# Kernel tuning notes

Measured on AMD Instinct MI355X. Metric: run time of the kernel, lower is better.

Reference implementation:

```python
import jax, jax.numpy as jnp
import numpy as np

N, E, D, L = 50000, 800000, 128, 3
BN_EPS = 1e-5

def setup_inputs() -> dict:
    key = jax.random.key(0)
    ks = jax.random.split(key, 6)
    x = jax.random.normal(ks[0], (N, D), dtype=jnp.float32)
    edge_index = jax.random.randint(ks[1], (2, E), 0, N, dtype=jnp.int64)
    W1 = jax.random.normal(ks[2], (L, D, D), dtype=jnp.float32) * (1.0 / np.sqrt(D))
    W2 = jax.random.normal(ks[3], (L, D, D), dtype=jnp.float32) * (1.0 / np.sqrt(D))
    return {
        'x': x, 'edge_index': edge_index,
        'W1': W1, 'b1': jnp.zeros((L, D), jnp.float32),
        'gamma': jnp.ones((L, D), jnp.float32), 'beta': jnp.zeros((L, D), jnp.float32),
        'bn_mean': jnp.zeros((L, D), jnp.float32), 'bn_var': jnp.ones((L, D), jnp.float32),
        'W2': W2, 'b2': jnp.zeros((L, D), jnp.float32),
        'eps': jnp.zeros((L,), jnp.float32),
    }

def reference(x, edge_index, W1, b1, gamma, beta, bn_mean, bn_var, W2, b2, eps):
    src, dst = edge_index[0], edge_index[1]
    h = x
    for l in range(L):
        # GIN aggregation: (1+eps)*h_i + sum_{j->i} h_j  (scatter-add over edges)
        agg = jax.ops.segment_sum(h[src], dst, num_segments=N)  # [N, D]
        z = (1.0 + eps[l]) * h + agg
        # MLP: Linear -> BatchNorm(eval, running stats) -> ReLU -> Linear
        z = z @ W1[l] + b1[l]
        z = (z - bn_mean[l]) * jax.lax.rsqrt(bn_var[l] + BN_EPS) * gamma[l] + beta[l]
        z = jax.nn.relu(z)
        z = z @ W2[l] + b2[l]
        if l < L - 1:
            z = jax.nn.relu(z)  # inter-layer ReLU; dropout is identity in eval
        h = z
    return h
```

## Files before the change

### kernel.cpp

```cpp
#include <hip/hip_runtime.h>
#include <hip/hip_fp16.h>

#define NN 50000
#define NE 800000
#define DD 128
#define NL 3
#define BN_EPS 1e-5f

#define NBIN 196
#define BCAP 5120
#define EB 4096
#define NB3 ((NE + EB - 1) / EB)

typedef short bf16x8 __attribute__((ext_vector_type(8)));
typedef float f32x4  __attribute__((ext_vector_type(4)));
typedef unsigned int u32x4 __attribute__((ext_vector_type(4)));


__device__ __forceinline__ unsigned int rne16(float v) {
    unsigned int u = __float_as_uint(v);
    return (u + 0x7fffu + ((u >> 16) & 1u)) >> 16;
}
__device__ __forceinline__ unsigned int packf(float v) {
    unsigned int hb = rne16(v);
    float hf = __uint_as_float(hb << 16);
    unsigned int lb = rne16(v - hf);
    return (hb << 16) | lb;
}
__device__ __forceinline__ float unpackf(unsigned int p) {
    return __uint_as_float(p & 0xffff0000u) + __uint_as_float(p << 16);
}


__global__ __launch_bounds__(256) void binscatter_kernel(
    const int* __restrict__ src, const int* __restrict__ dst,
    int* __restrict__ bin_cursor, uint2* __restrict__ binned) {
    __shared__ int lhist[NBIN];
    __shared__ int lbase[NBIN];
    __shared__ int lcur[NBIN];
    int t = threadIdx.x;
    for (int i = t; i < NBIN; i += 256) { lhist[i] = 0; lcur[i] = 0; }
    __syncthreads();
    int base = blockIdx.x * EB;
    int d[16], s[16], b[16];
#pragma unroll
    for (int i = 0; i < 16; ++i) {
        int e = base + t + i * 256;
        if (e < NE) {
            d[i] = dst[e]; s[i] = src[e]; b[i] = d[i] >> 8;
            atomicAdd(&lhist[b[i]], 1);
        } else b[i] = -1;
    }
    __syncthreads();
    for (int i = t; i < NBIN; i += 256) {
        int c = lhist[i];
        lbase[i] = c ? atomicAdd(&bin_cursor[i], c) : 0;
    }
    __syncthreads();
#pragma unroll
    for (int i = 0; i < 16; ++i)
        if (b[i] >= 0) {
            int p = lbase[b[i]] + atomicAdd(&lcur[b[i]], 1);
            binned[(size_t)b[i] * BCAP + p] = make_uint2((unsigned)s[i], (unsigned)d[i]);
        }
}

__global__ __launch_bounds__(256) void bincount_kernel(
    const uint2* __restrict__ binned, const int* __restrict__ bin_cursor,
    int* __restrict__ counts) {
    __shared__ int lcnt[256];
    int bI = blockIdx.x, t = threadIdx.x;
    lcnt[t] = 0;
    __syncthreads();
    int cnt = bin_cursor[bI];
    const uint2* be = binned + (size_t)bI * BCAP;
    for (int i = t; i < cnt; i += 256)
        atomicAdd(&lcnt[be[i].y & 255], 1);
    __syncthreads();
    int node = bI * 256 + t;
    if (node < NN) counts[node] = lcnt[t];
}

__global__ void scan1_kernel(const int* __restrict__ counts, int* __restrict__ otmp,
                             int* __restrict__ bsums) {
    __shared__ int sd[1024];
    int t = threadIdx.x;
    int i = blockIdx.x * 1024 + t;
    int v = (i < NN) ? counts[i] : 0;
    sd[t] = v; __syncthreads();
    for (int off = 1; off < 1024; off <<= 1) {
        int tmp = (t >= off) ? sd[t - off] : 0;
        __syncthreads();
        sd[t] += tmp;
        __syncthreads();
    }
    if (i < NN) otmp[i] = sd[t] - v;
    if (t == 1023) bsums[blockIdx.x] = sd[1023];
}

__global__ void scan2_kernel(const int* __restrict__ bsums, int* __restrict__ boffs, int nb) {
    __shared__ int sd[64];
    int t = threadIdx.x;
    int v = (t < nb) ? bsums[t] : 0;
    sd[t] = v; __syncthreads();
    for (int off = 1; off < 64; off <<= 1) {
        int tmp = (t >= off) ? sd[t - off] : 0;
        __syncthreads();
        sd[t] += tmp;
        __syncthreads();
    }
    if (t < nb) boffs[t] = sd[t] - v;
}

__global__ void scan3_kernel(const int* __restrict__ otmp, const int* __restrict__ boffs,
                             int* __restrict__ offsets) {
    int i = blockIdx.x * 1024 + threadIdx.x;
    if (i < NN) offsets[i] = otmp[i] + boffs[blockIdx.x];
}

__global__ __launch_bounds__(256) void binfill_kernel(
    const uint2* __restrict__ binned, const int* __restrict__ bin_cursor,
    const int* __restrict__ offs, int* __restrict__ csr) {
    __shared__ int lcur[256];
    int bI = blockIdx.x, t = threadIdx.x;
    lcur[t] = 0;
    __syncthreads();
    int cnt = bin_cursor[bI];
    const uint2* be = binned + (size_t)bI * BCAP;
    for (int i = t; i < cnt; i += 256) {
        uint2 e = be[i];
        int node = (int)e.y;
        int p = atomicAdd(&lcur[node & 255], 1);
        csr[offs[node] + p] = (int)e.x;
    }
}


__global__ void wsplit_kernel(const float* __restrict__ W1, const float* __restrict__ W2,
                              unsigned short* __restrict__ Whi, unsigned short* __restrict__ Wlo) {
    int idx = blockIdx.x * 256 + threadIdx.x;
    if (idx >= 6 * 16384) return;
    int m = idx >> 14;
    int r = idx & 16383;
    int n = r >> 7, k = r & 127;
    const float* Wsrc = (m < 3) ? (W1 + (size_t)m * 16384) : (W2 + (size_t)(m - 3) * 16384);
    float v = Wsrc[k * DD + n];
    unsigned int hb = rne16(v);
    float hf = __uint_as_float(hb << 16);
    unsigned int lb = rne16(v - hf);
    Whi[idx] = (unsigned short)hb;
    Wlo[idx] = (unsigned short)lb;
}


__global__ void tofp16_kernel(const float* __restrict__ x, unsigned int* __restrict__ x16) {
    int i = blockIdx.x * 256 + threadIdx.x;
    if (i >= NN * 64) return;
    float2 v = ((const float2*)x)[i];
    __half2 h = __float22half2_rn(v);
    x16[i] = __builtin_bit_cast(unsigned int, h);
}


template <bool SELF_F32>
__global__ __launch_bounds__(256) void agg_kernel(const void* __restrict__ selfv,
    const unsigned int* __restrict__ h16,
    const int* __restrict__ offsets, const int* __restrict__ counts,
    const int* __restrict__ csr, const float* __restrict__ eps, int l,
    unsigned int* __restrict__ aggp) {
    int wid = (int)((blockIdx.x * 256 + threadIdx.x) >> 6);
    int lane = threadIdx.x & 63;
    if (wid >= NN) return;
    float se = 1.0f + eps[l];
    float ax, ay;
    if (SELF_F32) {
        float2 s = ((const float2*)((const float*)selfv + (size_t)wid * DD))[lane];
        ax = s.x * se; ay = s.y * se;
    } else {
        uint2 s = ((const uint2*)((const unsigned int*)selfv + (size_t)wid * DD))[lane];
        ax = unpackf(s.x) * se; ay = unpackf(s.y) * se;
    }
    int e = offsets[wid];
    int end = e + counts[wid];
    for (; e + 8 <= end; e += 8) {
        int idx[8];
#pragma unroll
        for (int q = 0; q < 8; ++q) idx[q] = csr[e + q];
        unsigned int p[8];
#pragma unroll
        for (int q = 0; q < 8; ++q) p[q] = h16[(size_t)idx[q] * 64 + lane];
#pragma unroll
        for (int q = 0; q < 8; ++q) {
            float2 f = __half22float2(__builtin_bit_cast(__half2, p[q]));
            ax += f.x; ay += f.y;
        }
    }
    for (; e < end; ++e) {
        unsigned int p = h16[(size_t)csr[e] * 64 + lane];
        float2 f = __half22float2(__builtin_bit_cast(__half2, p));
        ax += f.x; ay += f.y;
    }
    uint2 o; o.x = packf(ax); o.y = packf(ay);
    ((uint2*)(aggp + (size_t)wid * DD))[lane] = o;
}


__device__ __forceinline__ void gemm_half(const unsigned int* Al, const bf16x8 (&wh)[4][2],
                                          const bf16x8 (&wl)[4][2], int lane,
                                          f32x4 (&acc)[4][2]) {
#pragma unroll
    for (int r = 0; r < 4; ++r) {
        int rl = r * 16 + (lane & 15);
        int sw = rl & 7;
#pragma unroll
        for (int kb = 0; kb < 4; ++kb) {
            int c0 = kb * 8 + ((lane >> 4) << 1);
            u32x4 q0 = *(const u32x4*)(&Al[rl * DD + ((c0 ^ sw) << 2)]);
            u32x4 q1 = *(const u32x4*)(&Al[rl * DD + (((c0 + 1) ^ sw) << 2)]);
            u32x4 hr, lr;
            hr.x = (q0.x >> 16) | (q0.y & 0xffff0000u);
            hr.y = (q0.z >> 16) | (q0.w & 0xffff0000u);
            hr.z = (q1.x >> 16) | (q1.y & 0xffff0000u);
            hr.w = (q1.z >> 16) | (q1.w & 0xffff0000u);
            lr.x = (q0.x & 0xffffu) | (q0.y << 16);
            lr.y = (q0.z & 0xffffu) | (q0.w << 16);
            lr.z = (q1.x & 0xffffu) | (q1.y << 16);
            lr.w = (q1.z & 0xffffu) | (q1.w << 16);
            bf16x8 ah = __builtin_bit_cast(bf16x8, hr);
            bf16x8 al = __builtin_bit_cast(bf16x8, lr);
#pragma unroll
            for (int nb = 0; nb < 2; ++nb) {
                acc[r][nb] = __builtin_amdgcn_mfma_f32_16x16x32_bf16(ah, wh[kb][nb], acc[r][nb], 0, 0, 0);
                acc[r][nb] = __builtin_amdgcn_mfma_f32_16x16x32_bf16(ah, wl[kb][nb], acc[r][nb], 0, 0, 0);
                acc[r][nb] = __builtin_amdgcn_mfma_f32_16x16x32_bf16(al, wh[kb][nb], acc[r][nb], 0, 0, 0);
            }
        }
    }
}

__global__ __launch_bounds__(256, 3) void mlp_kernel(
    const unsigned int* __restrict__ Ap,
    const unsigned short* __restrict__ Wh1, const unsigned short* __restrict__ Wl1,
    const unsigned short* __restrict__ Wh2, const unsigned short* __restrict__ Wl2,
    const float* __restrict__ b1v, const float* __restrict__ gamma,
    const float* __restrict__ beta, const float* __restrict__ mean,
    const float* __restrict__ var, const float* __restrict__ b2v,
    void* __restrict__ outp, unsigned short* __restrict__ out16, int last) {
    __shared__ unsigned int Al[64 * DD];
    int t = threadIdx.x;
    int lane = t & 63, w = t >> 6;
    int r0 = blockIdx.x * 64;
    int cb = w * 32;
    int nfrag = lane & 15;
    int kfrag = (lane >> 4) << 3;

    bf16x8 wh[4][2], wl[4][2];
#pragma unroll
    for (int kb = 0; kb < 4; ++kb)
#pragma unroll
        for (int nb = 0; nb < 2; ++nb) {
            size_t off = (size_t)(cb + nb * 16 + nfrag) * DD + kb * 32 + kfrag;
            wh[kb][nb] = *(const bf16x8*)(Wh1 + off);
            wl[kb][nb] = *(const bf16x8*)(Wl1 + off);
        }

    {
        int cchunk = t & 31;
#pragma unroll
        for (int it = 0; it < 8; ++it) {
            int rl = it * 8 + (t >> 5);
            int rg = r0 + rl; if (rg > NN - 1) rg = NN - 1;
            u32x4 v = *(const u32x4*)(Ap + (size_t)rg * DD + cchunk * 4);
            *(u32x4*)(&Al[rl * DD + ((cchunk ^ (rl & 7)) << 2)]) = v;
        }
    }
    __syncthreads();

    f32x4 acc[4][2];
#pragma unroll
    for (int r = 0; r < 4; ++r)
#pragma unroll
        for (int nb = 0; nb < 2; ++nb) acc[r][nb] = (f32x4){0.f, 0.f, 0.f, 0.f};

    gemm_half(Al, wh, wl, lane, acc);

#pragma unroll
    for (int kb = 0; kb < 4; ++kb)
#pragma unroll
        for (int nb = 0; nb < 2; ++nb) {
            size_t off = (size_t)(cb + nb * 16 + nfrag) * DD + kb * 32 + kfrag;
            wh[kb][nb] = *(const bf16x8*)(Wh2 + off);
            wl[kb][nb] = *(const bf16x8*)(Wl2 + off);
        }

    __syncthreads();

#pragma unroll
    for (int nb = 0; nb < 2; ++nb) {
        int col = cb + nb * 16 + nfrag;
        float bs = b1v[col];
        float iv = rsqrtf(var[col] + BN_EPS);
        float sc = iv * gamma[col];
        float sh = beta[col] - mean[col] * sc;
#pragma unroll
        for (int r = 0; r < 4; ++r)
#pragma unroll
            for (int j = 0; j < 4; ++j) {
                int row = r * 16 + ((lane >> 4) << 2) + j;
                float v = fmaxf(fmaf(acc[r][nb][j] + bs, sc, sh), 0.0f);
                Al[row * DD + ((((col >> 2) ^ (row & 7)) << 2) | (col & 3))] = packf(v);
            }
    }
    __syncthreads();

#pragma unroll
    for (int r = 0; r < 4; ++r)
#pragma unroll
        for (int nb = 0; nb < 2; ++nb) acc[r][nb] = (f32x4){0.f, 0.f, 0.f, 0.f};

    gemm_half(Al, wh, wl, lane, acc);

#pragma unroll
    for (int nb = 0; nb < 2; ++nb) {
        int col = cb + nb * 16 + nfrag;
        float bs = b2v[col];
#pragma unroll
        for (int r = 0; r < 4; ++r)
#pragma unroll
            for (int j = 0; j < 4; ++j) {
                int orow = r0 + r * 16 + ((lane >> 4) << 2) + j;
                if (orow < NN) {
                    float v = acc[r][nb][j] + bs;
                    if (last) {
                        ((float*)outp)[(size_t)orow * DD + col] = v;
                    } else {
                        v = fmaxf(v, 0.0f);
                        ((unsigned int*)outp)[(size_t)orow * DD + col] = packf(v);
                        out16[(size_t)orow * DD + col] =
                            __builtin_bit_cast(unsigned short, __float2half_rn(v));
                    }
                }
            }
    }
}


extern "C" void kernel_launch(void* const* d_in, const int* in_sizes, int n_in,
                              void* d_out, int out_size, void* d_ws, size_t ws_size,
                              hipStream_t stream) {
    const float* x     = (const float*)d_in[0];
    const int*   eidx  = (const int*)d_in[1];
    const float* W1    = (const float*)d_in[2];
    const float* b1    = (const float*)d_in[3];
    const float* gamma = (const float*)d_in[4];
    const float* beta  = (const float*)d_in[5];
    const float* bnm   = (const float*)d_in[6];
    const float* bnv   = (const float*)d_in[7];
    const float* W2    = (const float*)d_in[8];
    const float* b2    = (const float*)d_in[9];
    const float* eps   = (const float*)d_in[10];
    float* out = (float*)d_out;

    const int* src = eidx;
    const int* dst = eidx + NE;

    char* wsp = (char*)d_ws;
    unsigned int* bufA = (unsigned int*)wsp;  wsp += (size_t)NN * DD * 4;
    unsigned int* bufB = (unsigned int*)wsp;  wsp += (size_t)NN * DD * 4;
    unsigned int* x16  = (unsigned int*)wsp;  wsp += (size_t)NN * DD * 2;
    unsigned int* h16  = (unsigned int*)wsp;  wsp += (size_t)NN * DD * 2;
    uint2* binned      = (uint2*)wsp;         wsp += (size_t)NBIN * BCAP * 8;
    int* csr    = (int*)wsp;                  wsp += (size_t)NE * 4;
    int* counts = (int*)wsp;                  wsp += (size_t)NN * 4;
    int* offs   = (int*)wsp;                  wsp += (size_t)NN * 4;
    int* bin_cursor = (int*)wsp;              wsp += (size_t)NBIN * 4;
    unsigned short* Whi = (unsigned short*)wsp; wsp += (size_t)6 * 16384 * 2;
    unsigned short* Wlo = (unsigned short*)wsp; wsp += (size_t)6 * 16384 * 2;
    int* bsums  = (int*)wsp;                  wsp += 64 * 4;
    int* boffs  = (int*)wsp;                  wsp += 64 * 4;

    hipMemsetAsync(bin_cursor, 0, (size_t)NBIN * 4, stream);

    wsplit_kernel<<<(6 * 16384 + 255) / 256, 256, 0, stream>>>(W1, W2, Whi, Wlo);
    tofp16_kernel<<<(NN * 64 + 255) / 256, 256, 0, stream>>>(x, x16);

    int nbScan = (NN + 1023) / 1024;
    binscatter_kernel<<<NB3, 256, 0, stream>>>(src, dst, bin_cursor, binned);
    bincount_kernel<<<NBIN, 256, 0, stream>>>(binned, bin_cursor, counts);
    scan1_kernel<<<nbScan, 1024, 0, stream>>>(counts, offs, bsums);
    scan2_kernel<<<1, 64, 0, stream>>>(bsums, boffs, nbScan);
    scan3_kernel<<<nbScan, 1024, 0, stream>>>(offs, boffs, offs);
    binfill_kernel<<<NBIN, 256, 0, stream>>>(binned, bin_cursor, offs, csr);

    int aggBlocks = (NN * 64 + 255) / 256;
    int mlpBlocks = (NN + 63) / 64;

    for (int l = 0; l < NL; ++l) {
        if (l == 0)
            agg_kernel<true><<<aggBlocks, 256, 0, stream>>>(x, x16, offs, counts, csr, eps, l, bufA);
        else
            agg_kernel<false><<<aggBlocks, 256, 0, stream>>>(bufB, h16, offs, counts, csr, eps, l, bufA);
        int last = (l == NL - 1);
        mlp_kernel<<<mlpBlocks, 256, 0, stream>>>(
            bufA,
            Whi + (size_t)l * 16384, Wlo + (size_t)l * 16384,
            Whi + (size_t)(3 + l) * 16384, Wlo + (size_t)(3 + l) * 16384,
            b1 + (size_t)l * DD, gamma + (size_t)l * DD, beta + (size_t)l * DD,
            bnm + (size_t)l * DD, bnv + (size_t)l * DD, b2 + (size_t)l * DD,
            last ? (void*)out : (void*)bufB, (unsigned short*)h16, last);
    }
}
```

Baseline: 364.2 us.

## Halve MLP row tile, widen CSR build blocks, merge prep kernels

The MLP kernel now handles 32 rows per block instead of 64. That halves its shared-memory tile and accumulators, so the launch bound can ask for 5 blocks per CU, and the grid doubles in size. The bin scatter, count and fill kernels move to 1024-thread blocks, giving more parallelism per bin in the preprocessing stage. The weight-split and fp16-conversion kernels are merged into one launch to cut launch overhead. The cost is that each block reuses the register-resident weights over fewer rows, so weight loads are amortised less.

```diff
diff --git a/kernel.cpp b/kernel.cpp
--- a/kernel.cpp
+++ b/kernel.cpp
@@ -32,53 +32,53 @@
 }
 
 
-__global__ __launch_bounds__(256) void binscatter_kernel(
+__global__ __launch_bounds__(1024) void binscatter_kernel(
     const int* __restrict__ src, const int* __restrict__ dst,
     int* __restrict__ bin_cursor, uint2* __restrict__ binned) {
     __shared__ int lhist[NBIN];
     __shared__ int lbase[NBIN];
     __shared__ int lcur[NBIN];
     int t = threadIdx.x;
-    for (int i = t; i < NBIN; i += 256) { lhist[i] = 0; lcur[i] = 0; }
+    for (int i = t; i < NBIN; i += 1024) { lhist[i] = 0; lcur[i] = 0; }
     __syncthreads();
     int base = blockIdx.x * EB;
-    int d[16], s[16], b[16];
-#pragma unroll
-    for (int i = 0; i < 16; ++i) {
-        int e = base + t + i * 256;
+    int d[4], s[4], b[4];
+#pragma unroll
+    for (int i = 0; i < 4; ++i) {
+        int e = base + t + i * 1024;
         if (e < NE) {
             d[i] = dst[e]; s[i] = src[e]; b[i] = d[i] >> 8;
             atomicAdd(&lhist[b[i]], 1);
         } else b[i] = -1;
     }
     __syncthreads();
-    for (int i = t; i < NBIN; i += 256) {
+    for (int i = t; i < NBIN; i += 1024) {
         int c = lhist[i];
         lbase[i] = c ? atomicAdd(&bin_cursor[i], c) : 0;
     }
     __syncthreads();
 #pragma unroll
-    for (int i = 0; i < 16; ++i)
+    for (int i = 0; i < 4; ++i)
         if (b[i] >= 0) {
             int p = lbase[b[i]] + atomicAdd(&lcur[b[i]], 1);
             binned[(size_t)b[i] * BCAP + p] = make_uint2((unsigned)s[i], (unsigned)d[i]);
         }
 }
 
-__global__ __launch_bounds__(256) void bincount_kernel(
+__global__ __launch_bounds__(1024) void bincount_kernel(
     const uint2* __restrict__ binned, const int* __restrict__ bin_cursor,
     int* __restrict__ counts) {
     __shared__ int lcnt[256];
     int bI = blockIdx.x, t = threadIdx.x;
-    lcnt[t] = 0;
+    if (t < 256) lcnt[t] = 0;
     __syncthreads();
     int cnt = bin_cursor[bI];
     const uint2* be = binned + (size_t)bI * BCAP;
-    for (int i = t; i < cnt; i += 256)
+    for (int i = t; i < cnt; i += 1024)
         atomicAdd(&lcnt[be[i].y & 255], 1);
     __syncthreads();
     int node = bI * 256 + t;
-    if (node < NN) counts[node] = lcnt[t];
+    if (t < 256 && node < NN) counts[node] = lcnt[t];
 }
 
 __global__ void scan1_kernel(const int* __restrict__ counts, int* __restrict__ otmp,
@@ -118,16 +118,16 @@
     if (i < NN) offsets[i] = otmp[i] + boffs[blockIdx.x];
 }
 
-__global__ __launch_bounds__(256) void binfill_kernel(
+__global__ __launch_bounds__(1024) void binfill_kernel(
     const uint2* __restrict__ binned, const int* __restrict__ bin_cursor,
     const int* __restrict__ offs, int* __restrict__ csr) {
     __shared__ int lcur[256];
     int bI = blockIdx.x, t = threadIdx.x;
-    lcur[t] = 0;
+    if (t < 256) lcur[t] = 0;
     __syncthreads();
     int cnt = bin_cursor[bI];
     const uint2* be = binned + (size_t)bI * BCAP;
-    for (int i = t; i < cnt; i += 256) {
+    for (int i = t; i < cnt; i += 1024) {
         uint2 e = be[i];
         int node = (int)e.y;
         int p = atomicAdd(&lcur[node & 255], 1);
@@ -136,29 +136,27 @@
 }
 
 
-__global__ void wsplit_kernel(const float* __restrict__ W1, const float* __restrict__ W2,
-                              unsigned short* __restrict__ Whi, unsigned short* __restrict__ Wlo) {
+__global__ void prep_kernel(const float* __restrict__ W1, const float* __restrict__ W2,
+                            unsigned short* __restrict__ Whi, unsigned short* __restrict__ Wlo,
+                            const float* __restrict__ x, unsigned int* __restrict__ x16) {
     int idx = blockIdx.x * 256 + threadIdx.x;
-    if (idx >= 6 * 16384) return;
-    int m = idx >> 14;
-    int r = idx & 16383;
-    int n = r >> 7, k = r & 127;
-    const float* Wsrc = (m < 3) ? (W1 + (size_t)m * 16384) : (W2 + (size_t)(m - 3) * 16384);
-    float v = Wsrc[k * DD + n];
-    unsigned int hb = rne16(v);
-    float hf = __uint_as_float(hb << 16);
-    unsigned int lb = rne16(v - hf);
-    Whi[idx] = (unsigned short)hb;
-    Wlo[idx] = (unsigned short)lb;
-}
-
-
-__global__ void tofp16_kernel(const float* __restrict__ x, unsigned int* __restrict__ x16) {
-    int i = blockIdx.x * 256 + threadIdx.x;
-    if (i >= NN * 64) return;
-    float2 v = ((const float2*)x)[i];
-    __half2 h = __float22half2_rn(v);
-    x16[i] = __builtin_bit_cast(unsigned int, h);
+    if (idx < 6 * 16384) {
+        int m = idx >> 14;
+        int r = idx & 16383;
+        int n = r >> 7, k = r & 127;
+        const float* Wsrc = (m < 3) ? (W1 + (size_t)m * 16384) : (W2 + (size_t)(m - 3) * 16384);
+        float v = Wsrc[k * DD + n];
+        unsigned int hb = rne16(v);
+        float hf = __uint_as_float(hb << 16);
+        unsigned int lb = rne16(v - hf);
+        Whi[idx] = (unsigned short)hb;
+        Wlo[idx] = (unsigned short)lb;
+    }
+    if (idx < NN * 64) {
+        float2 v = ((const float2*)x)[idx];
+        __half2 h = __float22half2_rn(v);
+        x16[idx] = __builtin_bit_cast(unsigned int, h);
+    }
 }
 
 
@@ -205,11 +203,11 @@
 }
 
 
-__device__ __forceinline__ void gemm_half(const unsigned int* Al, const bf16x8 (&wh)[4][2],
-                                          const bf16x8 (&wl)[4][2], int lane,
-                                          f32x4 (&acc)[4][2]) {
-#pragma unroll
-    for (int r = 0; r < 4; ++r) {
+__device__ __forceinline__ void gemm_half32(const unsigned int* Al, const bf16x8 (&wh)[4][2],
+                                            const bf16x8 (&wl)[4][2], int lane,
+                                            f32x4 (&acc)[2][2]) {
+#pragma unroll
+    for (int r = 0; r < 2; ++r) {
         int rl = r * 16 + (lane & 15);
         int sw = rl & 7;
 #pragma unroll
@@ -238,7 +236,7 @@
     }
 }
 
-__global__ __launch_bounds__(256, 3) void mlp_kernel(
+__global__ __launch_bounds__(256, 5) void mlp_kernel(
     const unsigned int* __restrict__ Ap,
     const unsigned short* __restrict__ Wh1, const unsigned short* __restrict__ Wl1,
     const unsigned short* __restrict__ Wh2, const unsigned short* __restrict__ Wl2,
@@ -246,10 +244,10 @@
     const float* __restrict__ beta, const float* __restrict__ mean,
     const float* __restrict__ var, const float* __restrict__ b2v,
     void* __restrict__ outp, unsigned short* __restrict__ out16, int last) {
-    __shared__ unsigned int Al[64 * DD];
+    __shared__ unsigned int Al[32 * DD];
     int t = threadIdx.x;
     int lane = t & 63, w = t >> 6;
-    int r0 = blockIdx.x * 64;
+    int r0 = blockIdx.x * 32;
     int cb = w * 32;
     int nfrag = lane & 15;
     int kfrag = (lane >> 4) << 3;
@@ -267,7 +265,7 @@
     {
         int cchunk = t & 31;
 #pragma unroll
-        for (int it = 0; it < 8; ++it) {
+        for (int it = 0; it < 4; ++it) {
             int rl = it * 8 + (t >> 5);
             int rg = r0 + rl; if (rg > NN - 1) rg = NN - 1;
             u32x4 v = *(const u32x4*)(Ap + (size_t)rg * DD + cchunk * 4);
@@ -276,13 +274,13 @@
     }
     __syncthreads();
 
-    f32x4 acc[4][2];
-#pragma unroll
-    for (int r = 0; r < 4; ++r)
+    f32x4 acc[2][2];
+#pragma unroll
+    for (int r = 0; r < 2; ++r)
 #pragma unroll
         for (int nb = 0; nb < 2; ++nb) acc[r][nb] = (f32x4){0.f, 0.f, 0.f, 0.f};
 
-    gemm_half(Al, wh, wl, lane, acc);
+    gemm_half32(Al, wh, wl, lane, acc);
 
 #pragma unroll
     for (int kb = 0; kb < 4; ++kb)
@@ -303,7 +301,7 @@
         float sc = iv * gamma[col];
         float sh = beta[col] - mean[col] * sc;
 #pragma unroll
-        for (int r = 0; r < 4; ++r)
+        for (int r = 0; r < 2; ++r)
 #pragma unroll
             for (int j = 0; j < 4; ++j) {
                 int row = r * 16 + ((lane >> 4) << 2) + j;
@@ -314,18 +312,18 @@
     __syncthreads();
 
 #pragma unroll
-    for (int r = 0; r < 4; ++r)
+    for (int r = 0; r < 2; ++r)
 #pragma unroll
         for (int nb = 0; nb < 2; ++nb) acc[r][nb] = (f32x4){0.f, 0.f, 0.f, 0.f};
 
-    gemm_half(Al, wh, wl, lane, acc);
+    gemm_half32(Al, wh, wl, lane, acc);
 
 #pragma unroll
     for (int nb = 0; nb < 2; ++nb) {
         int col = cb + nb * 16 + nfrag;
         float bs = b2v[col];
 #pragma unroll
-        for (int r = 0; r < 4; ++r)
+        for (int r = 0; r < 2; ++r)
 #pragma unroll
             for (int j = 0; j < 4; ++j) {
                 int orow = r0 + r * 16 + ((lane >> 4) << 2) + j;
@@ -381,19 +379,18 @@
 
     hipMemsetAsync(bin_cursor, 0, (size_t)NBIN * 4, stream);
 
-    wsplit_kernel<<<(6 * 16384 + 255) / 256, 256, 0, stream>>>(W1, W2, Whi, Wlo);
-    tofp16_kernel<<<(NN * 64 + 255) / 256, 256, 0, stream>>>(x, x16);
+    prep_kernel<<<(NN * 64 + 255) / 256, 256, 0, stream>>>(W1, W2, Whi, Wlo, x, x16);
 
     int nbScan = (NN + 1023) / 1024;
-    binscatter_kernel<<<NB3, 256, 0, stream>>>(src, dst, bin_cursor, binned);
-    bincount_kernel<<<NBIN, 256, 0, stream>>>(binned, bin_cursor, counts);
+    binscatter_kernel<<<NB3, 1024, 0, stream>>>(src, dst, bin_cursor, binned);
+    bincount_kernel<<<NBIN, 1024, 0, stream>>>(binned, bin_cursor, counts);
     scan1_kernel<<<nbScan, 1024, 0, stream>>>(counts, offs, bsums);
     scan2_kernel<<<1, 64, 0, stream>>>(bsums, boffs, nbScan);
     scan3_kernel<<<nbScan, 1024, 0, stream>>>(offs, boffs, offs);
-    binfill_kernel<<<NBIN, 256, 0, stream>>>(binned, bin_cursor, offs, csr);
+    binfill_kernel<<<NBIN, 1024, 0, stream>>>(binned, bin_cursor, offs, csr);
 
     int aggBlocks = (NN * 64 + 255) / 256;
-    int mlpBlocks = (NN + 63) / 64;
+    int mlpBlocks = (NN + 31) / 32;
 
     for (int l = 0; l < NL; ++l) {
         if (l == 0)
```

After: 434.4 us. +19.3%, slower.
